# Performance work log

Hardware: AMD Instinct MI355X
Metric: run time of the kernel (lower is better)

The kernel has to match this reference:

```python
import jax, jax.numpy as jnp
import numpy as np

TEMPERATURE = 0.07
TIME_THRESH = 5.0 * 1e6  # microseconds


def setup_inputs() -> dict:
    key = jax.random.key(0)
    k1, k2, k3 = jax.random.split(key, 3)
    B, D = 8192, 512
    desc = jax.random.normal(k1, (B, D), dtype=jnp.float32)
    desc = desc / jnp.linalg.norm(desc, axis=-1, keepdims=True)  # module expects normalized descriptors
    seq_ids = jax.random.randint(k2, (B,), 0, 64, dtype=jnp.int64)
    time_mid = jax.random.randint(k3, (B,), 0, 20_000_000, dtype=jnp.int64)
    return {"descriptors": desc, "seq_ids": seq_ids, "time_mid": time_mid}


def reference(descriptors, seq_ids, time_mid):
    B = descriptors.shape[0]
    # [B, B] temperature-scaled cosine similarities
    logits = jnp.matmul(descriptors, descriptors.T) / TEMPERATURE

    eye = jnp.eye(B, dtype=bool)
    same_seq = seq_ids[:, None] == seq_ids[None, :]
    close_time = jnp.abs(time_mid[:, None] - time_mid[None, :]).astype(jnp.float32) < TIME_THRESH
    pos_mask = same_seq & close_time & ~eye  # positives
    offdiag = ~eye                            # positives + negatives = denominator support

    # denominator per row i: log sum_{j != i} exp(logits[i, j])
    denom_lse = jax.nn.logsumexp(jnp.where(offdiag, logits, -jnp.inf), axis=1)  # [B]

    # per positive pair (i, j): -log( exp(l_ij) / denom_i ) = denom_lse_i - l_ij
    pair_loss = jnp.where(pos_mask, denom_lse[:, None] - logits, 0.0)
    num_pos = jnp.sum(pos_mask)
    loss = jnp.sum(pair_loss) / jnp.maximum(num_pos, 1).astype(pair_loss.dtype)
    return loss
```

## Files before the change

### kernel.cpp

```cpp
#include <hip/hip_runtime.h>
#include <math.h>

#define TILE 128

typedef __attribute__((ext_vector_type(4))) float f32x4;
typedef __attribute__((ext_vector_type(2))) long long llong2;

#define INV_T    14.285714285714286f
#define K2C      20.60992915f
#define K2C8     0.32203014296875f
#define INV_T64  0.22321428571428573f
#define TIME_THR 5000000

__device__ __forceinline__ unsigned pack_bf16x2(float lo, float hi) {
  unsigned a = __float_as_uint(lo);
  unsigned b = __float_as_uint(hi);
  a = (a + 0x7FFFu + ((a >> 16) & 1u)) >> 16;
  b = (b + 0x7FFFu + ((b >> 16) & 1u)) & 0xFFFF0000u;
  return b | a;
}

__device__ __forceinline__ unsigned f32_to_e4m3(float x) {
  unsigned u = __float_as_uint(x);
  unsigned s = (u >> 24) & 0x80u;
  int e = (int)((u >> 23) & 0xffu) - 127;
  unsigned m = u & 0x7fffffu;
  if (e < -9) return s;
  if (e < -6) {
    int sh = 20 + (-6 - e);
    unsigned full = (1u << 23) | m;
    unsigned q = full >> sh;
    unsigned rem = full & ((1u << sh) - 1u);
    unsigned half = 1u << (sh - 1);
    if (rem > half || (rem == half && (q & 1u))) q++;
    return s | q;
  }
  unsigned q = m >> 20;
  unsigned rem = m & 0xfffffu;
  if (rem > 0x80000u || (rem == 0x80000u && (q & 1u))) q++;
  int ee = e;
  if (q == 8u) { q = 0u; ee++; }
  if (ee > 8 || (ee == 8 && q == 7u)) return s | 0x7eu;
  return s | (unsigned)((ee + 7) << 3) | q;
}

__device__ __forceinline__ void gl_lds16(const void* g, void* l) {
  __builtin_amdgcn_global_load_lds(
      (const __attribute__((address_space(1))) unsigned int*)g,
      (__attribute__((address_space(3))) unsigned int*)l, 16, 0, 0);
}

template <int MODE>
__device__ __forceinline__ void infonce_body(
    const float* __restrict__ desc, const unsigned char* __restrict__ desc8,
    const int* __restrict__ seq, const int* __restrict__ tmid,
    float* __restrict__ p_se, float* __restrict__ p_ps,
    float* __restrict__ p_pc, int B, int D, int NB) {
  __shared__ __align__(16) unsigned char lA8[2][TILE][128];
  __shared__ __align__(16) unsigned char lB8[2][TILE][128];
  __shared__ int mseq_r[TILE], mtim_r[TILE], mseq_c[TILE], mtim_c[TILE];

  const int T = NB * (NB + 1) / 2;
  int t = blockIdx.x;
  if ((T & 7) == 0) t = (t & 7) * (T >> 3) + (t >> 3);
  float fn = (float)NB + 0.5f;
  int r = (int)(fn - sqrtf(fmaxf(fn * fn - 2.0f * (float)t, 0.0f)));
  if (r < 0) r = 0;
  if (r > NB - 1) r = NB - 1;
  auto Sf = [NB](int rr) { return rr * NB - ((rr * (rr - 1)) >> 1); };
  while (r > 0 && Sf(r) > t) --r;
  while (r < NB - 1 && Sf(r + 1) <= t) ++r;
  const int rb = r;
  const int cb = rb + (t - Sf(rb));
  const bool upper = (cb != rb);

  const int row0 = rb * TILE;
  const int col0 = cb * TILE;

  const int tid = threadIdx.x;
  const int l = tid & 63;
  const int w = tid >> 6;
  const int wrow = (w >> 1) << 6;
  const int wcol = (w & 1) << 6;
  const int lr = l & 15;
  const int kg = l >> 4;

  if (tid < TILE) {
    mseq_r[tid] = seq[row0 + tid];
    mtim_r[tid] = tmid[row0 + tid];
    mseq_c[tid] = seq[col0 + tid];
    mtim_c[tid] = tmid[col0 + tid];
  }

  f32x4 acc[4][4];
#pragma unroll
  for (int m = 0; m < 4; ++m)
#pragma unroll
    for (int n = 0; n < 4; ++n) acc[m][n] = (f32x4){0.f, 0.f, 0.f, 0.f};

  const int sr = tid >> 3;
  const int sc = tid & 7;

  if (MODE == 2) {
    const int NT = D >> 7;
    const unsigned char* pa =
        desc8 + (size_t)(row0 + (tid >> 3)) * D + (tid & 7) * 16;
    const unsigned char* pb =
        desc8 + (size_t)(col0 + (tid >> 3)) * D + (tid & 7) * 16;
    const size_t rstep = (size_t)32 * D;

    auto stage = [&](int bu_, int tt) {
      const int off = tt << 7;
#pragma unroll
      for (int q = 0; q < 4; ++q) {
        gl_lds16(pa + (size_t)q * rstep + off,
                 (char*)&lA8[bu_][0][0] + (q << 12) + tid * 16);
        gl_lds16(pb + (size_t)q * rstep + off,
                 (char*)&lB8[bu_][0][0] + (q << 12) + tid * 16);
      }
    };

    __builtin_amdgcn_sched_barrier(0);
    stage(0, 0);
    __builtin_amdgcn_sched_barrier(0);

    for (int ts = 0; ts < NT; ++ts) {
      const int bu = ts & 1;
      if (ts + 1 < NT) {
        stage(bu ^ 1, ts + 1);
        __builtin_amdgcn_sched_barrier(0);
        asm volatile("s_waitcnt vmcnt(8)" ::: "memory");
      } else {
        asm volatile("s_waitcnt vmcnt(0)" ::: "memory");
      }
      __builtin_amdgcn_sched_barrier(0);
      __builtin_amdgcn_s_barrier();
      __builtin_amdgcn_sched_barrier(0);

      llong2 av[4][2], bv[4][2];
#pragma unroll
      for (int m = 0; m < 4; ++m) {
        const int row = wrow + (m << 4) + lr;
#pragma unroll
        for (int j2 = 0; j2 < 2; ++j2) {
          const int ch = ((j2 << 2) + kg) ^ (row & 7);
          av[m][j2] =
              *reinterpret_cast<const llong2*>(&lA8[bu][row][ch << 4]);
        }
      }
#pragma unroll
      for (int n = 0; n < 4; ++n) {
        const int row = wcol + (n << 4) + lr;
#pragma unroll
        for (int j2 = 0; j2 < 2; ++j2) {
          const int ch = ((j2 << 2) + kg) ^ (row & 7);
          bv[n][j2] =
              *reinterpret_cast<const llong2*>(&lB8[bu][row][ch << 4]);
        }
      }
      __builtin_amdgcn_sched_barrier(0);
      asm volatile("s_waitcnt lgkmcnt(0)" ::: "memory");
      __builtin_amdgcn_sched_barrier(0);
      __builtin_amdgcn_s_setprio(1);
#pragma unroll
      for (int j2 = 0; j2 < 2; ++j2)
#pragma unroll
        for (int kk = 0; kk < 2; ++kk)
#pragma unroll
          for (int m = 0; m < 4; ++m)
#pragma unroll
            for (int n = 0; n < 4; ++n)
              acc[m][n] = __builtin_amdgcn_mfma_f32_16x16x32_fp8_fp8(
                  av[m][j2][kk], bv[n][j2][kk], acc[m][n], 0, 0, 0);
      __builtin_amdgcn_s_setprio(0);
      __builtin_amdgcn_sched_barrier(0);
      __builtin_amdgcn_s_barrier();
    }
    __syncthreads();
  } else {
    __shared__ __align__(16) unsigned short lAw[TILE][64];
    __shared__ __align__(16) unsigned short lBw[TILE][64];
    typedef __attribute__((ext_vector_type(8))) short short8v;
    for (int k0 = 0; k0 < D; k0 += 64) {
      __syncthreads();
#pragma unroll
      for (int p = 0; p < 4; ++p) {
        const int rr = (p << 5) + sr;
        const float* gA = desc + (size_t)(row0 + rr) * D + k0 + (sc << 3);
        const float4 fa0 = *reinterpret_cast<const float4*>(gA);
        const float4 fa1 = *reinterpret_cast<const float4*>(gA + 4);
        const float* gB = desc + (size_t)(col0 + rr) * D + k0 + (sc << 3);
        const float4 fb0 = *reinterpret_cast<const float4*>(gB);
        const float4 fb1 = *reinterpret_cast<const float4*>(gB + 4);
        uint4 wa, wb;
        wa.x = pack_bf16x2(fa0.x, fa0.y);
        wa.y = pack_bf16x2(fa0.z, fa0.w);
        wa.z = pack_bf16x2(fa1.x, fa1.y);
        wa.w = pack_bf16x2(fa1.z, fa1.w);
        wb.x = pack_bf16x2(fb0.x, fb0.y);
        wb.y = pack_bf16x2(fb0.z, fb0.w);
        wb.z = pack_bf16x2(fb1.x, fb1.y);
        wb.w = pack_bf16x2(fb1.z, fb1.w);
        const int dst = (sc ^ (rr & 7)) << 3;
        *reinterpret_cast<uint4*>(&lAw[rr][dst]) = wa;
        *reinterpret_cast<uint4*>(&lBw[rr][dst]) = wb;
      }
      __syncthreads();
#pragma unroll
      for (int kk = 0; kk < 2; ++kk) {
        short8v af[4], bf[4];
#pragma unroll
        for (int m = 0; m < 4; ++m) {
          const int rowa = wrow + (m << 4) + lr;
          const int ch = ((kk << 2) + kg) ^ (rowa & 7);
          af[m] = *reinterpret_cast<const short8v*>(&lAw[rowa][ch << 3]);
        }
#pragma unroll
        for (int n = 0; n < 4; ++n) {
          const int rowb = wcol + (n << 4) + lr;
          const int ch = ((kk << 2) + kg) ^ (rowb & 7);
          bf[n] = *reinterpret_cast<const short8v*>(&lBw[rowb][ch << 3]);
        }
#pragma unroll
        for (int m = 0; m < 4; ++m)
#pragma unroll
          for (int n = 0; n < 4; ++n)
            acc[m][n] = __builtin_amdgcn_mfma_f32_16x16x32_bf16(af[m], bf[n],
                                                                acc[m][n], 0, 0, 0);
      }
    }
    __syncthreads();
  }

  float* rowred = (float*)&lA8[0][0][0];
  float* colred = (float*)&lB8[0][0][0];

  const float kmul = (MODE == 2) ? K2C8 : K2C;
  const float psc = (MODE == 2) ? INV_T64 : INV_T;

  int cseq[4], ctim[4], gcol[4];
#pragma unroll
  for (int n = 0; n < 4; ++n) {
    const int cl = wcol + (n << 4) + lr;
    cseq[n] = mseq_c[cl];
    ctim[n] = mtim_c[cl];
    gcol[n] = col0 + cl;
  }
  float colse[4] = {0.f, 0.f, 0.f, 0.f};
  float colpd[4] = {0.f, 0.f, 0.f, 0.f};
  float colpc[4] = {0.f, 0.f, 0.f, 0.f};

#pragma unroll
  for (int m = 0; m < 4; ++m) {
#pragma unroll
    for (int reg = 0; reg < 4; ++reg) {
      const int rl = wrow + (m << 4) + (kg << 2) + reg;
      const int growg = row0 + rl;
      const int rs = mseq_r[rl];
      const int rt = mtim_r[rl];
      float se = 0.f, pd = 0.f, pcnt = 0.f;
#pragma unroll
      for (int n = 0; n < 4; ++n) {
        const float dot = acc[m][n][reg];
        const float e = exp2f(fmaf(dot, kmul, -K2C));
        const bool nd = (growg != gcol[n]);
        int dt = rt - ctim[n];
        dt = dt < 0 ? -dt : dt;
        const bool pos = nd && (rs == cseq[n]) && (dt < TIME_THR);
        const float ev = nd ? e : 0.f;
        const float dv = pos ? dot : 0.f;
        const float cv = pos ? 1.f : 0.f;
        se += ev;
        pd += dv;
        pcnt += cv;
        if (upper) {
          colse[n] += ev;
          colpd[n] += dv;
          colpc[n] += cv;
        }
      }
#pragma unroll
      for (int s = 1; s < 16; s <<= 1) {
        se += __shfl_xor(se, s);
        pd += __shfl_xor(pd, s);
        pcnt += __shfl_xor(pcnt, s);
      }
      if ((l & 15) == 0) {
        if (MODE == 2) {
          const int half = wcol >> 6;
          float* rr3 = rowred + ((size_t)(half * TILE + rl)) * 3;
          rr3[0] = se;
          rr3[1] = pd;
          rr3[2] = pcnt;
        } else {
          atomicAdd(&p_se[growg], se);
          atomicAdd(&p_ps[growg], pd * psc);
          atomicAdd(&p_pc[growg], pcnt);
        }
      }
    }
  }
  if (upper) {
#pragma unroll
    for (int n = 0; n < 4; ++n) {
      float cs = colse[n], cp = colpd[n], cc = colpc[n];
      cs += __shfl_xor(cs, 16);
      cp += __shfl_xor(cp, 16);
      cc += __shfl_xor(cc, 16);
      cs += __shfl_xor(cs, 32);
      cp += __shfl_xor(cp, 32);
      cc += __shfl_xor(cc, 32);
      if (kg == 0) {
        if (MODE == 2) {
          const int half = wrow >> 6;
          const int cl = wcol + (n << 4) + lr;
          float* cr3 = colred + ((size_t)(half * TILE + cl)) * 3;
          cr3[0] = cs;
          cr3[1] = cp;
          cr3[2] = cc;
        } else {
          atomicAdd(&p_se[gcol[n]], cs);
          atomicAdd(&p_ps[gcol[n]], cp * psc);
          atomicAdd(&p_pc[gcol[n]], cc);
        }
      }
    }
  }

  if (MODE == 2) {
    __syncthreads();
    if (tid < TILE) {
      const int row = tid;
      const float se = rowred[(size_t)row * 3 + 0] + rowred[(size_t)(TILE + row) * 3 + 0];
      const float pd = rowred[(size_t)row * 3 + 1] + rowred[(size_t)(TILE + row) * 3 + 1];
      const float pc = rowred[(size_t)row * 3 + 2] + rowred[(size_t)(TILE + row) * 3 + 2];
      const size_t o = (size_t)cb * B + row0 + row;
      p_se[o] = se;
      p_ps[o] = pd * INV_T64;
      p_pc[o] = pc;
    } else if (upper && tid < 2 * TILE) {
      const int col = tid - TILE;
      const float se = colred[(size_t)col * 3 + 0] + colred[(size_t)(TILE + col) * 3 + 0];
      const float pd = colred[(size_t)col * 3 + 1] + colred[(size_t)(TILE + col) * 3 + 1];
      const float pc = colred[(size_t)col * 3 + 2] + colred[(size_t)(TILE + col) * 3 + 2];
      const size_t o = (size_t)rb * B + col0 + col;
      p_se[o] = se;
      p_ps[o] = pd * INV_T64;
      p_pc[o] = pc;
    }
  }
}

__global__ __launch_bounds__(256, 2) void infonce_main2(
    const float* desc, const unsigned char* desc8, const int* seq,
    const int* tmid, float* p_se, float* p_ps, float* p_pc, int B, int D,
    int NB) {
  infonce_body<2>(desc, desc8, seq, tmid, p_se, p_ps, p_pc, B, D, NB);
}
__global__ __launch_bounds__(256, 2) void infonce_main0(
    const float* desc, const unsigned char* desc8, const int* seq,
    const int* tmid, float* p_se, float* p_ps, float* p_pc, int B, int D,
    int NB) {
  infonce_body<0>(desc, desc8, seq, tmid, p_se, p_ps, p_pc, B, D, NB);
}

__global__ __launch_bounds__(256) void conv_fp8(const float* __restrict__ in,
                                                unsigned char* __restrict__ out,
                                                int D, int nchunk) {
  const int u = blockIdx.x * 256 + threadIdx.x;
  if (u >= nchunk) return;
  const int cpr = D >> 4;
  const int r = u / cpr;
  const int cc = u - r * cpr;
  const int kt = cc >> 3;
  const int p = cc & 7;
  const int g = p ^ (r & 7);
  const int j2 = g >> 2;
  const int kgc = g & 3;
  const float* src = in + (size_t)r * D + (kt << 7) + (j2 << 6) + (kgc << 3);
  const float4 f0 = *reinterpret_cast<const float4*>(src);
  const float4 f1 = *reinterpret_cast<const float4*>(src + 4);
  const float4 g0 = *reinterpret_cast<const float4*>(src + 32);
  const float4 g1 = *reinterpret_cast<const float4*>(src + 36);
  unsigned char b[16];
  b[0] = f32_to_e4m3(f0.x * 8.f);
  b[1] = f32_to_e4m3(f0.y * 8.f);
  b[2] = f32_to_e4m3(f0.z * 8.f);
  b[3] = f32_to_e4m3(f0.w * 8.f);
  b[4] = f32_to_e4m3(f1.x * 8.f);
  b[5] = f32_to_e4m3(f1.y * 8.f);
  b[6] = f32_to_e4m3(f1.z * 8.f);
  b[7] = f32_to_e4m3(f1.w * 8.f);
  b[8] = f32_to_e4m3(g0.x * 8.f);
  b[9] = f32_to_e4m3(g0.y * 8.f);
  b[10] = f32_to_e4m3(g0.z * 8.f);
  b[11] = f32_to_e4m3(g0.w * 8.f);
  b[12] = f32_to_e4m3(g1.x * 8.f);
  b[13] = f32_to_e4m3(g1.y * 8.f);
  b[14] = f32_to_e4m3(g1.z * 8.f);
  b[15] = f32_to_e4m3(g1.w * 8.f);
  uint4 wv;
  unsigned* wp = (unsigned*)&wv;
#pragma unroll
  for (int d = 0; d < 4; ++d)
    wp[d] = (unsigned)b[d * 4] | ((unsigned)b[d * 4 + 1] << 8) |
            ((unsigned)b[d * 4 + 2] << 16) | ((unsigned)b[d * 4 + 3] << 24);
  *reinterpret_cast<uint4*>(out + (size_t)u * 16) = wv;
}

__global__ __launch_bounds__(256) void reduce_parts4(
    const float* __restrict__ p_se, const float* __restrict__ p_ps,
    const float* __restrict__ p_pc, float* __restrict__ bnum,
    float* __restrict__ bcnt, int B, int NB) {
  const int tid = threadIdx.x;
  const int rloc = tid & 63;
  const int chunk = tid >> 6;
  const int row = blockIdx.x * 64 + rloc;
  const int jpc = NB >> 2;
  float se = 0.f, ps = 0.f, pc = 0.f;
  for (int j = chunk * jpc; j < (chunk + 1) * jpc; ++j) {
    const size_t o = (size_t)j * B + row;
    se += p_se[o];
    ps += p_ps[o];
    pc += p_pc[o];
  }
  __shared__ float s3[3][4][64];
  s3[0][chunk][rloc] = se;
  s3[1][chunk][rloc] = ps;
  s3[2][chunk][rloc] = pc;
  __syncthreads();
  if (tid < 64) {
    const float tse = s3[0][0][tid] + s3[0][1][tid] + s3[0][2][tid] + s3[0][3][tid];
    const float tps = s3[1][0][tid] + s3[1][1][tid] + s3[1][2][tid] + s3[1][3][tid];
    const float tpc = s3[2][0][tid] + s3[2][1][tid] + s3[2][2][tid] + s3[2][3][tid];
    float a = tpc * (logf(tse) + INV_T) - tps;
    float b = tpc;
#pragma unroll
    for (int s = 1; s < 64; s <<= 1) {
      a += __shfl_xor(a, s);
      b += __shfl_xor(b, s);
    }
    if (tid == 0) {
      bnum[blockIdx.x] = a;
      bcnt[blockIdx.x] = b;
    }
  }
}

__global__ __launch_bounds__(256) void final_reduce(
    const float* __restrict__ bnum, const float* __restrict__ bcnt,
    float* __restrict__ out, int n) {
  __shared__ float sn[256];
  __shared__ float sc[256];
  const int tid = threadIdx.x;
  float a = 0.f, b = 0.f;
  for (int i = tid; i < n; i += 256) {
    a += bnum[i];
    b += bcnt[i];
  }
  sn[tid] = a;
  sc[tid] = b;
  __syncthreads();
  for (int s = 128; s > 0; s >>= 1) {
    if (tid < s) {
      sn[tid] += sn[tid + s];
      sc[tid] += sc[tid + s];
    }
    __syncthreads();
  }
  if (tid == 0) out[0] = sn[0] / fmaxf(sc[0], 1.f);
}

__global__ __launch_bounds__(1024) void infonce_finalize(
    const float* __restrict__ a_se, const float* __restrict__ a_ps,
    const float* __restrict__ a_pc, float* __restrict__ out, int B) {
  __shared__ float sn[1024];
  __shared__ float sc[1024];
  const int tid = threadIdx.x;
  float num = 0.f, cnt = 0.f;
  for (int i = tid; i < B; i += 1024) {
    const float c = a_pc[i];
    num += c * (logf(a_se[i]) + INV_T) - a_ps[i];
    cnt += c;
  }
  sn[tid] = num;
  sc[tid] = cnt;
  __syncthreads();
  for (int s = 512; s > 0; s >>= 1) {
    if (tid < s) {
      sn[tid] += sn[tid + s];
      sc[tid] += sc[tid + s];
    }
    __syncthreads();
  }
  if (tid == 0) out[0] = sn[0] / fmaxf(sc[0], 1.f);
}

extern "C" void kernel_launch(void* const* d_in, const int* in_sizes, int n_in,
                              void* d_out, int out_size, void* d_ws, size_t ws_size,
                              hipStream_t stream) {
  (void)n_in;
  (void)out_size;
  const float* desc = (const float*)d_in[0];
  const int* seq = (const int*)d_in[1];
  const int* tmid = (const int*)d_in[2];
  const int B = in_sizes[1];
  const int D = in_sizes[0] / B;
  const int NB = B / TILE;
  const int T = NB * (NB + 1) / 2;

  const size_t desc8_bytes = (size_t)B * D;
  const size_t parts_elems = (size_t)B * NB;
  const size_t nb1 = (size_t)B / 64;
  const size_t need8 = desc8_bytes + 3 * parts_elems * 4 + 2 * nb1 * 4;

  if ((B & 255) == 0 && (D & 127) == 0 && ws_size >= need8) {
    unsigned char* desc8 = (unsigned char*)d_ws;
    float* p_se = (float*)((char*)d_ws + desc8_bytes);
    float* p_ps = p_se + parts_elems;
    float* p_pc = p_ps + parts_elems;
    float* bnum = p_pc + parts_elems;
    float* bcnt = bnum + nb1;
    const int nchunk = (int)(((size_t)B * D) >> 4);
    conv_fp8<<<(nchunk + 255) / 256, 256, 0, stream>>>(desc, desc8, D, nchunk);
    infonce_main2<<<T, 256, 0, stream>>>(desc, desc8, seq, tmid, p_se, p_ps,
                                         p_pc, B, D, NB);
    const int nrb = B / 64;
    reduce_parts4<<<nrb, 256, 0, stream>>>(p_se, p_ps, p_pc, bnum, bcnt, B, NB);
    final_reduce<<<1, 256, 0, stream>>>(bnum, bcnt, (float*)d_out, nrb);
  } else {
    float* a_se = (float*)d_ws;
    float* a_ps = a_se + B;
    float* a_pc = a_ps + B;
    hipMemsetAsync(d_ws, 0, (size_t)3 * B * sizeof(float), stream);
    infonce_main0<<<T, 256, 0, stream>>>(desc, nullptr, seq, tmid, a_se, a_ps,
                                         a_pc, B, D, NB);
    infonce_finalize<<<1, 1024, 0, stream>>>(a_se, a_ps, a_pc, (float*)d_out, B);
  }
}
```

Baseline: 95.47 us.

## Single-buffer B tile in FP8 path to fit three blocks per CU

New measurement: 109.7 us. +15.0%, slower.

```diff
diff --git a/kernel.cpp b/kernel.cpp
--- a/kernel.cpp
+++ b/kernel.cpp
@@ -56,10 +56,6 @@
     const int* __restrict__ seq, const int* __restrict__ tmid,
     float* __restrict__ p_se, float* __restrict__ p_ps,
     float* __restrict__ p_pc, int B, int D, int NB) {
-  __shared__ __align__(16) unsigned char lA8[2][TILE][128];
-  __shared__ __align__(16) unsigned char lB8[2][TILE][128];
-  __shared__ int mseq_r[TILE], mtim_r[TILE], mseq_c[TILE], mtim_c[TILE];
-
   const int T = NB * (NB + 1) / 2;
   int t = blockIdx.x;
   if ((T & 7) == 0) t = (t & 7) * (T >> 3) + (t >> 3);
@@ -85,13 +81,6 @@
   const int lr = l & 15;
   const int kg = l >> 4;
 
-  if (tid < TILE) {
-    mseq_r[tid] = seq[row0 + tid];
-    mtim_r[tid] = tmid[row0 + tid];
-    mseq_c[tid] = seq[col0 + tid];
-    mtim_c[tid] = tmid[col0 + tid];
-  }
-
   f32x4 acc[4][4];
 #pragma unroll
   for (int m = 0; m < 4; ++m)
@@ -102,6 +91,17 @@
   const int sc = tid & 7;
 
   if (MODE == 2) {
+    __shared__ __align__(16) unsigned char lA8[2][TILE][128];
+    __shared__ __align__(16) unsigned char lB8[TILE][128];
+    __shared__ int mseq_r[TILE], mtim_r[TILE], mseq_c[TILE], mtim_c[TILE];
+
+    if (tid < TILE) {
+      mseq_r[tid] = seq[row0 + tid];
+      mtim_r[tid] = tmid[row0 + tid];
+      mseq_c[tid] = seq[col0 + tid];
+      mtim_c[tid] = tmid[col0 + tid];
+    }
+
     const int NT = D >> 7;
     const unsigned char* pa =
         desc8 + (size_t)(row0 + (tid >> 3)) * D + (tid & 7) * 16;
@@ -109,27 +109,32 @@
         desc8 + (size_t)(col0 + (tid >> 3)) * D + (tid & 7) * 16;
     const size_t rstep = (size_t)32 * D;
 
-    auto stage = [&](int bu_, int tt) {
+    auto stageA = [&](int bu_, int tt) {
       const int off = tt << 7;
 #pragma unroll
-      for (int q = 0; q < 4; ++q) {
+      for (int q = 0; q < 4; ++q)
         gl_lds16(pa + (size_t)q * rstep + off,
                  (char*)&lA8[bu_][0][0] + (q << 12) + tid * 16);
+    };
+    auto stageB = [&](int tt) {
+      const int off = tt << 7;
+#pragma unroll
+      for (int q = 0; q < 4; ++q)
         gl_lds16(pb + (size_t)q * rstep + off,
-                 (char*)&lB8[bu_][0][0] + (q << 12) + tid * 16);
-      }
+                 (char*)&lB8[0][0] + (q << 12) + tid * 16);
     };
 
     __builtin_amdgcn_sched_barrier(0);
-    stage(0, 0);
+    stageA(0, 0);
+    stageB(0);
     __builtin_amdgcn_sched_barrier(0);
 
     for (int ts = 0; ts < NT; ++ts) {
       const int bu = ts & 1;
       if (ts + 1 < NT) {
-        stage(bu ^ 1, ts + 1);
+        stageA(bu ^ 1, ts + 1);
         __builtin_amdgcn_sched_barrier(0);
-        asm volatile("s_waitcnt vmcnt(8)" ::: "memory");
+        asm volatile("s_waitcnt vmcnt(4)" ::: "memory");
       } else {
         asm volatile("s_waitcnt vmcnt(0)" ::: "memory");
       }
@@ -154,8 +159,7 @@
 #pragma unroll
         for (int j2 = 0; j2 < 2; ++j2) {
           const int ch = ((j2 << 2) + kg) ^ (row & 7);
-          bv[n][j2] =
-              *reinterpret_cast<const llong2*>(&lB8[bu][row][ch << 4]);
+          bv[n][j2] = *reinterpret_cast<const llong2*>(&lB8[row][ch << 4]);
         }
       }
       __builtin_amdgcn_sched_barrier(0);
@@ -175,12 +179,128 @@
       __builtin_amdgcn_s_setprio(0);
       __builtin_amdgcn_sched_barrier(0);
       __builtin_amdgcn_s_barrier();
+      __builtin_amdgcn_sched_barrier(0);
+      if (ts + 1 < NT) stageB(ts + 1);
+      __builtin_amdgcn_sched_barrier(0);
     }
     __syncthreads();
+
+    float* rowred = (float*)&lA8[0][0][0];
+    float* colred = (float*)&lB8[0][0];
+
+    int cseq[4], ctim[4], gcol[4];
+#pragma unroll
+    for (int n = 0; n < 4; ++n) {
+      const int cl = wcol + (n << 4) + lr;
+      cseq[n] = mseq_c[cl];
+      ctim[n] = mtim_c[cl];
+      gcol[n] = col0 + cl;
+    }
+    float colse[4] = {0.f, 0.f, 0.f, 0.f};
+    float colpd[4] = {0.f, 0.f, 0.f, 0.f};
+    float colpc[4] = {0.f, 0.f, 0.f, 0.f};
+
+#pragma unroll
+    for (int m = 0; m < 4; ++m) {
+#pragma unroll
+      for (int reg = 0; reg < 4; ++reg) {
+        const int rl = wrow + (m << 4) + (kg << 2) + reg;
+        const int growg = row0 + rl;
+        const int rs = mseq_r[rl];
+        const int rt = mtim_r[rl];
+        float se = 0.f, pd = 0.f, pcnt = 0.f;
+#pragma unroll
+        for (int n = 0; n < 4; ++n) {
+          const float dot = acc[m][n][reg];
+          const float e = exp2f(fmaf(dot, K2C8, -K2C));
+          const bool nd = (growg != gcol[n]);
+          int dt = rt - ctim[n];
+          dt = dt < 0 ? -dt : dt;
+          const bool pos = nd && (rs == cseq[n]) && (dt < TIME_THR);
+          const float ev = nd ? e : 0.f;
+          const float dv = pos ? dot : 0.f;
+          const float cv = pos ? 1.f : 0.f;
+          se += ev;
+          pd += dv;
+          pcnt += cv;
+          colse[n] += ev;
+          colpd[n] += dv;
+          colpc[n] += cv;
+        }
+#pragma unroll
+        for (int s = 1; s < 16; s <<= 1) {
+          se += __shfl_xor(se, s);
+          pd += __shfl_xor(pd, s);
+          pcnt += __shfl_xor(pcnt, s);
+        }
+        if (lr == 0) {
+          const int half = wcol >> 6;
+          float* rr3 = rowred + ((size_t)(half * TILE + rl)) * 3;
+          rr3[0] = se;
+          rr3[1] = pd;
+          rr3[2] = pcnt;
+        }
+      }
+    }
+    if (upper) {
+#pragma unroll
+      for (int n = 0; n < 4; ++n) {
+        float cs = colse[n], cp = colpd[n], cc = colpc[n];
+        cs += __shfl_xor(cs, 16);
+        cp += __shfl_xor(cp, 16);
+        cc += __shfl_xor(cc, 16);
+        cs += __shfl_xor(cs, 32);
+        cp += __shfl_xor(cp, 32);
+        cc += __shfl_xor(cc, 32);
+        if (l < 16) {
+          const int half = wrow >> 6;
+          const int cl = wcol + (n << 4) + lr;
+          float* cr3 = colred + ((size_t)(half * TILE + cl)) * 3;
+          cr3[0] = cs;
+          cr3[1] = cp;
+          cr3[2] = cc;
+        }
+      }
+    }
+    __syncthreads();
+
+    if (tid < TILE) {
+      const int row = tid;
+      const float se =
+          rowred[(size_t)row * 3 + 0] + rowred[(size_t)(TILE + row) * 3 + 0];
+      const float pd =
+          rowred[(size_t)row * 3 + 1] + rowred[(size_t)(TILE + row) * 3 + 1];
+      const float pc =
+          rowred[(size_t)row * 3 + 2] + rowred[(size_t)(TILE + row) * 3 + 2];
+      const size_t o = (size_t)cb * B + row0 + row;
+      p_se[o] = se;
+      p_ps[o] = pd * INV_T64;
+      p_pc[o] = pc;
+    } else if (upper && tid < 2 * TILE) {
+      const int col = tid - TILE;
+      const float se =
+          colred[(size_t)col * 3 + 0] + colred[(size_t)(TILE + col) * 3 + 0];
+      const float pd =
+          colred[(size_t)col * 3 + 1] + colred[(size_t)(TILE + col) * 3 + 1];
+      const float pc =
+          colred[(size_t)col * 3 + 2] + colred[(size_t)(TILE + col) * 3 + 2];
+      const size_t o = (size_t)rb * B + col0 + col;
+      p_se[o] = se;
+      p_ps[o] = pd * INV_T64;
+      p_pc[o] = pc;
+    }
   } else {
     __shared__ __align__(16) unsigned short lAw[TILE][64];
     __shared__ __align__(16) unsigned short lBw[TILE][64];
+    __shared__ int mseq_r[TILE], mtim_r[TILE], mseq_c[TILE], mtim_c[TILE];
     typedef __attribute__((ext_vector_type(8))) short short8v;
+
+    if (tid < TILE) {
+      mseq_r[tid] = seq[row0 + tid];
+      mtim_r[tid] = tmid[row0 + tid];
+      mseq_c[tid] = seq[col0 + tid];
+      mtim_c[tid] = tmid[col0 + tid];
+    }
     for (int k0 = 0; k0 < D; k0 += 64) {
       __syncthreads();
 #pragma unroll
@@ -230,128 +350,82 @@
       }
     }
     __syncthreads();
-  }
-
-  float* rowred = (float*)&lA8[0][0][0];
-  float* colred = (float*)&lB8[0][0][0];
-
-  const float kmul = (MODE == 2) ? K2C8 : K2C;
-  const float psc = (MODE == 2) ? INV_T64 : INV_T;
-
-  int cseq[4], ctim[4], gcol[4];
-#pragma unroll
-  for (int n = 0; n < 4; ++n) {
-    const int cl = wcol + (n << 4) + lr;
-    cseq[n] = mseq_c[cl];
-    ctim[n] = mtim_c[cl];
-    gcol[n] = col0 + cl;
-  }
-  float colse[4] = {0.f, 0.f, 0.f, 0.f};
-  float colpd[4] = {0.f, 0.f, 0.f, 0.f};
-  float colpc[4] = {0.f, 0.f, 0.f, 0.f};
-
-#pragma unroll
-  for (int m = 0; m < 4; ++m) {
-#pragma unroll
-    for (int reg = 0; reg < 4; ++reg) {
-      const int rl = wrow + (m << 4) + (kg << 2) + reg;
-      const int growg = row0 + rl;
-      const int rs = mseq_r[rl];
-      const int rt = mtim_r[rl];
-      float se = 0.f, pd = 0.f, pcnt = 0.f;
+
+    int cseq[4], ctim[4], gcol[4];
+#pragma unroll
+    for (int n = 0; n < 4; ++n) {
+      const int cl = wcol + (n << 4) + lr;
+      cseq[n] = mseq_c[cl];
+      ctim[n] = mtim_c[cl];
+      gcol[n] = col0 + cl;
+    }
+    float colse[4] = {0.f, 0.f, 0.f, 0.f};
+    float colpd[4] = {0.f, 0.f, 0.f, 0.f};
+    float colpc[4] = {0.f, 0.f, 0.f, 0.f};
+
+#pragma unroll
+    for (int m = 0; m < 4; ++m) {
+#pragma unroll
+      for (int reg = 0; reg < 4; ++reg) {
+        const int rl = wrow + (m << 4) + (kg << 2) + reg;
+        const int growg = row0 + rl;
+        const int rs = mseq_r[rl];
+        const int rt = mtim_r[rl];
+        float se = 0.f, pd = 0.f, pcnt = 0.f;
+#pragma unroll
+        for (int n = 0; n < 4; ++n) {
+          const float dot = acc[m][n][reg];
+          const float e = exp2f(fmaf(dot, K2C, -K2C));
+          const bool nd = (growg != gcol[n]);
+          int dt = rt - ctim[n];
+          dt = dt < 0 ? -dt : dt;
+          const bool pos = nd && (rs == cseq[n]) && (dt < TIME_THR);
+          const float ev = nd ? e : 0.f;
+          const float dv = pos ? dot : 0.f;
+          const float cv = pos ? 1.f : 0.f;
+          se += ev;
+          pd += dv;
+          pcnt += cv;
+          if (upper) {
+            colse[n] += ev;
+            colpd[n] += dv;
+            colpc[n] += cv;
+          }
+        }
+#pragma unroll
+        for (int s = 1; s < 16; s <<= 1) {
+          se += __shfl_xor(se, s);
+          pd += __shfl_xor(pd, s);
+          pcnt += __shfl_xor(pcnt, s);
+        }
+        if ((l & 15) == 0) {
+          atomicAdd(&p_se[growg], se);
+          atomicAdd(&p_ps[growg], pd * INV_T);
+          atomicAdd(&p_pc[growg], pcnt);
+        }
+      }
+    }
+    if (upper) {
 #pragma unroll
       for (int n = 0; n < 4; ++n) {
-        const float dot = acc[m][n][reg];
-        const float e = exp2f(fmaf(dot, kmul, -K2C));
-        const bool nd = (growg != gcol[n]);
-        int dt = rt - ctim[n];
-        dt = dt < 0 ? -dt : dt;
-        const bool pos = nd && (rs == cseq[n]) && (dt < TIME_THR);
-        const float ev = nd ? e : 0.f;
-        const float dv = pos ? dot : 0.f;
-        const float cv = pos ? 1.f : 0.f;
-        se += ev;
-        pd += dv;
-        pcnt += cv;
-        if (upper) {
-          colse[n] += ev;
-          colpd[n] += dv;
-          colpc[n] += cv;
-        }
-      }
-#pragma unroll
-      for (int s = 1; s < 16; s <<= 1) {
-        se += __shfl_xor(se, s);
-        pd += __shfl_xor(pd, s);
-        pcnt += __shfl_xor(pcnt, s);
-      }
-      if ((l & 15) == 0) {
-        if (MODE == 2) {
-          const int half = wcol >> 6;
-          float* rr3 = rowred + ((size_t)(half * TILE + rl)) * 3;
-          rr3[0] = se;
-          rr3[1] = pd;
-          rr3[2] = pcnt;
-        } else {
-          atomicAdd(&p_se[growg], se);
-          atomicAdd(&p_ps[growg], pd * psc);
-          atomicAdd(&p_pc[growg], pcnt);
-        }
-      }
-    }
-  }
-  if (upper) {
-#pragma unroll
-    for (int n = 0; n < 4; ++n) {
-      float cs = colse[n], cp = colpd[n], cc = colpc[n];
-      cs += __shfl_xor(cs, 16);
-      cp += __shfl_xor(cp, 16);
-      cc += __shfl_xor(cc, 16);
-      cs += __shfl_xor(cs, 32);
-      cp += __shfl_xor(cp, 32);
-      cc += __shfl_xor(cc, 32);
-      if (kg == 0) {
-        if (MODE == 2) {
-          const int half = wrow >> 6;
-          const int cl = wcol + (n << 4) + lr;
-          float* cr3 = colred + ((size_t)(half * TILE + cl)) * 3;
-          cr3[0] = cs;
-          cr3[1] = cp;
-          cr3[2] = cc;
-        } else {
+        float cs = colse[n], cp = colpd[n], cc = colpc[n];
+        cs += __shfl_xor(cs, 16);
+        cp += __shfl_xor(cp, 16);
+        cc += __shfl_xor(cc, 16);
+        cs += __shfl_xor(cs, 32);
+        cp += __shfl_xor(cp, 32);
+        cc += __shfl_xor(cc, 32);
+        if (kg == 0) {
           atomicAdd(&p_se[gcol[n]], cs);
-          atomicAdd(&p_ps[gcol[n]], cp * psc);
+          atomicAdd(&p_ps[gcol[n]], cp * INV_T);
           atomicAdd(&p_pc[gcol[n]], cc);
         }
       }
     }
   }
-
-  if (MODE == 2) {
-    __syncthreads();
-    if (tid < TILE) {
-      const int row = tid;
-      const float se = rowred[(size_t)row * 3 + 0] + rowred[(size_t)(TILE + row) * 3 + 0];
-      const float pd = rowred[(size_t)row * 3 + 1] + rowred[(size_t)(TILE + row) * 3 + 1];
-      const float pc = rowred[(size_t)row * 3 + 2] + rowred[(size_t)(TILE + row) * 3 + 2];
-      const size_t o = (size_t)cb * B + row0 + row;
-      p_se[o] = se;
-      p_ps[o] = pd * INV_T64;
-      p_pc[o] = pc;
-    } else if (upper && tid < 2 * TILE) {
-      const int col = tid - TILE;
-      const float se = colred[(size_t)col * 3 + 0] + colred[(size_t)(TILE + col) * 3 + 0];
-      const float pd = colred[(size_t)col * 3 + 1] + colred[(size_t)(TILE + col) * 3 + 1];
-      const float pc = colred[(size_t)col * 3 + 2] + colred[(size_t)(TILE + col) * 3 + 2];
-      const size_t o = (size_t)rb * B + col0 + col;
-      p_se[o] = se;
-      p_ps[o] = pd * INV_T64;
-      p_pc[o] = pc;
-    }
-  }
-}
-
-__global__ __launch_bounds__(256, 2) void infonce_main2(
+}
+
+__global__ __launch_bounds__(256, 3) void infonce_main2(
     const float* desc, const unsigned char* desc8, const int* seq,
     const int* tmid, float* p_se, float* p_ps, float* p_pc, int B, int D,
     int NB) {
```
